# Kernel tuning notes

Hardware: AMD Instinct MI355X
Metric: run time of the kernel (lower is better)

The kernel has to match this reference:

```python
import jax, jax.numpy as jnp
import numpy as np

HW, B, C, NH, NC, HF, WF = 2500, 2, 256, 8, 6, 64, 176
DFF = 4 * C
EPS = 1e-5

def _layernorm(x, g, b):
    m = x.mean(-1, keepdims=True)
    v = ((x - m) ** 2).mean(-1, keepdims=True)
    return (x - m) / jnp.sqrt(v + EPS) * g + b

def _mha(q, kv, in_w, in_b, ow, ob):
    # q: [L,B,C], kv: [S,B,C] (batch_first=False, torch nn.MultiheadAttention)
    L, Bq, Cq = q.shape
    S = kv.shape[0]
    Dh = Cq // NH
    qp = (q @ in_w[:Cq].T + in_b[:Cq]).reshape(L, Bq, NH, Dh)
    kp = (kv @ in_w[Cq:2 * Cq].T + in_b[Cq:2 * Cq]).reshape(S, Bq, NH, Dh)
    vp = (kv @ in_w[2 * Cq:].T + in_b[2 * Cq:]).reshape(S, Bq, NH, Dh)
    att = jnp.einsum('lbhd,sbhd->bhls', qp, kp) * (1.0 / np.sqrt(Dh))
    att = jax.nn.softmax(att, axis=-1)
    out = jnp.einsum('bhls,sbhd->lbhd', att, vp).reshape(L, Bq, Cq)
    return out @ ow.T + ob

def _grid_sample_zeros(feat, grid):
    # feat: [B,N,C,H,W], grid: [B,N,Q,2] in [-1,1]; bilinear, align_corners=False, zero padding
    Bb, N, Cc, Hf, Wf = feat.shape
    Q = grid.shape[2]
    x = (grid[..., 0] + 1.0) * (Wf / 2.0) - 0.5
    y = (grid[..., 1] + 1.0) * (Hf / 2.0) - 0.5
    x0 = jnp.floor(x); y0 = jnp.floor(y)
    wx = x - x0; wy = y - y0
    x0i = x0.astype(jnp.int32); y0i = y0.astype(jnp.int32)
    ff = feat.reshape(Bb, N, Cc, Hf * Wf)
    def corner(xi, yi, w):
        valid = (xi >= 0) & (xi < Wf) & (yi >= 0) & (yi < Hf)
        idx = jnp.clip(yi, 0, Hf - 1) * Wf + jnp.clip(xi, 0, Wf - 1)  # [B,N,Q]
        g = jnp.take_along_axis(ff, jnp.broadcast_to(idx[:, :, None, :], (Bb, N, Cc, Q)), axis=-1)
        return g * (w * valid)[:, :, None, :]
    return (corner(x0i, y0i, (1.0 - wx) * (1.0 - wy)) + corner(x0i + 1, y0i, wx * (1.0 - wy))
            + corner(x0i, y0i + 1, (1.0 - wx) * wy) + corner(x0i + 1, y0i + 1, wx * wy))

def _forward(bev_queries, prev_bev, image_feat, reference_points, camera_intrinsics, camera_extrinsics,
             in_proj_w, in_proj_b, out_proj_w, out_proj_b, tsa_norm_g, tsa_norm_b,
             sca_w, sca_b, sca_norm_g, sca_norm_b, ffn_w1, ffn_b1, ffn_w2, ffn_b2, ffn_norm_g, ffn_norm_b):
    # TSA (dropout is identity in eval)
    tsa_out = _mha(bev_queries, prev_bev, in_proj_w, in_proj_b, out_proj_w, out_proj_b)
    x = _layernorm(bev_queries + tsa_out, tsa_norm_g, tsa_norm_b)
    # SCA: ego->camera->image projection
    R = camera_extrinsics[:, :, :3, :3]            # [B,N,3,3]
    t = camera_extrinsics[:, :, :3, 3]             # [B,N,3]
    R_e2c = jnp.swapaxes(R, -1, -2)
    t_e2c = -jnp.einsum('bnij,bnj->bni', R_e2c, t)
    pts_cam = jnp.einsum('bnij,qj->bnqi', R_e2c, reference_points) + t_e2c[:, :, None, :]  # [B,N,Q,3]
    pts_img = jnp.einsum('bnij,bnqj->bnqi', camera_intrinsics, pts_cam)
    uv = pts_img[..., :2] / jnp.maximum(pts_img[..., 2:3], 1e-5)
    grid = jnp.stack([2.0 * uv[..., 0] / WF - 1.0, 2.0 * uv[..., 1] / HF - 1.0], axis=-1)  # [B,N,Q,2]
    Bq = bev_queries.shape[1]
    feat_r = image_feat.reshape(Bq, NC, C, HF, WF)
    sampled = _grid_sample_zeros(feat_r, grid).mean(axis=1)   # [B,C,Q]
    sampled = jnp.transpose(sampled, (2, 0, 1))               # [Q,B,C]
    sca_out = sampled @ sca_w.T + sca_b
    x = _layernorm(x + sca_out, sca_norm_g, sca_norm_b)
    # FFN (torch nn.GELU default = exact erf)
    h = jax.nn.gelu(x @ ffn_w1 + ffn_b1, approximate=False)
    ffn_out = h @ ffn_w2 + ffn_b2
    return _layernorm(x + ffn_out, ffn_norm_g, ffn_norm_b)

def setup_inputs():
    key = jax.random.key(0)
    ks = jax.random.split(key, 16)
    f = jnp.float32
    s = 0.02
    return {
        'bev_queries': jax.random.normal(ks[0], (HW, B, C), f),
        'prev_bev': jax.random.normal(ks[1], (HW, B, C), f),
        'image_feat': jax.random.normal(ks[2], (B * NC, C, HF, WF), f),
        'reference_points': jax.random.normal(ks[3], (HW, 3), f) * 20.0,
        'camera_intrinsics': jax.random.normal(ks[4], (B, NC, 3, 3), f),
        'camera_extrinsics': jax.random.normal(ks[5], (B, NC, 4, 4), f),
        'spatial_shapes': jnp.array([[HF, WF]], jnp.int32),
        'in_proj_w': jax.random.normal(ks[6], (3 * C, C), f) * s,
        'in_proj_b': jnp.zeros((3 * C,), f),
        'out_proj_w': jax.random.normal(ks[7], (C, C), f) * s,
        'out_proj_b': jnp.zeros((C,), f),
        'tsa_norm_g': jnp.ones((C,), f), 'tsa_norm_b': jnp.zeros((C,), f),
        'sca_w': jax.random.normal(ks[8], (C, C), f) * s,
        'sca_b': jnp.zeros((C,), f),
        'sca_norm_g': jnp.ones((C,), f), 'sca_norm_b': jnp.zeros((C,), f),
        'ffn_w1': jax.random.normal(ks[9], (C, DFF), f) * s,
        'ffn_b1': jnp.zeros((DFF,), f),
        'ffn_w2': jax.random.normal(ks[10], (DFF, C), f) * s,
        'ffn_b2': jnp.zeros((C,), f),
        'ffn_norm_g': jnp.ones((C,), f), 'ffn_norm_b': jnp.zeros((C,), f),
    }

def reference(bev_queries, prev_bev, image_feat, reference_points, camera_intrinsics, camera_extrinsics,
              in_proj_w, in_proj_b, out_proj_w, out_proj_b, tsa_norm_g, tsa_norm_b,
              sca_w, sca_b, sca_norm_g, sca_norm_b, ffn_w1, ffn_b1, ffn_w2, ffn_b2, ffn_norm_g, ffn_norm_b,
              spatial_shapes):
    return _forward(bev_queries, prev_bev, image_feat, reference_points, camera_intrinsics, camera_extrinsics,
                    in_proj_w, in_proj_b, out_proj_w, out_proj_b, tsa_norm_g, tsa_norm_b,
                    sca_w, sca_b, sca_norm_g, sca_norm_b, ffn_w1, ffn_b1, ffn_w2, ffn_b2, ffn_norm_g, ffn_norm_b)
```

## Files before the change

### kernel.cpp

```cpp
#include <hip/hip_runtime.h>

typedef unsigned short u16;
typedef __attribute__((ext_vector_type(8))) __bf16 bf8_t;
typedef __attribute__((ext_vector_type(4))) float f4_t;

union bf8u { u16 u[8]; bf8_t v; uint4 q; };

__device__ __forceinline__ float bf2f(u16 v) {
  return __uint_as_float(((unsigned int)v) << 16);
}
__device__ __forceinline__ u16 f2bf(float f) {
  union { __bf16 h; u16 u; } c;
  c.h = (__bf16)f;
  return c.u;
}
__device__ __forceinline__ float bflo(unsigned int w) { return __uint_as_float(w << 16); }
__device__ __forceinline__ float bfhi(unsigned int w) { return __uint_as_float(w & 0xFFFF0000u); }
__device__ __forceinline__ float ldf1(const void* p, size_t i, int isf32) {
  return isf32 ? ((const float*)p)[i] : bf2f(((const u16*)p)[i]);
}
__device__ __forceinline__ unsigned int cvtpk(float lo, float hi) {
  unsigned int w;
  asm("v_cvt_pk_bf16_f32 %0, %1, %2" : "=v"(w) : "v"(lo), "v"(hi));
  return w;
}

#define LQ    2500
#define LQP   2560
#define BB    2
#define CC    256
#define NCC   6
#define HFF   64
#define WFF   176
#define DFF   1024
#define MROWS 5000

#define WB_UV   256
#define WB_WQKV 240256
#define WB_WOP  633472
#define WB_WSC  764544
#define WB_WF1  895616
#define WB_WF2  1419904
#define WB_S1   1944192
#define WB_S2   (WB_S1 + 2621440)
#define WB_S3   (WB_S2 + 2621440)
#define WB_VT   (WB_S3 + 2621440)
#define WB_H    WB_S2

__global__ void detect_k(const u16* __restrict__ rp, int* __restrict__ flag) {
  int bad = 0;
  for (int i = threadIdx.x; i < 7500; i += 64) {
    float v = bf2f(rp[i]);
    if (!(fabsf(v) < 1e6f)) bad = 1;
  }
  int anybad = __any(bad);
  if (threadIdx.x == 0) flag[0] = anybad ? 1 : 0;
}

struct WDesc {
  const void* src[6];
  u16* dst[6];
  int n[6];
  int mode[6];
  int Kd[6], Nd[6];
};
__global__ __launch_bounds__(256) void cvtw_k(WDesc d,
    const void* __restrict__ refp, const void* __restrict__ intr,
    const void* __restrict__ extr, float* __restrict__ uv,
    const int* __restrict__ flag) {
  const int df = flag[0];
  const int i = blockIdx.y;
  if (i == 6) {
    for (int idx = blockIdx.x * 256 + threadIdx.x; idx < BB * NCC * LQ; idx += gridDim.x * 256) {
      const int bc = idx / LQ;
      const int q = idx - bc * LQ;
      float R[3][3], tv[3], Kc[3][3], p[3];
#pragma unroll
      for (int a = 0; a < 3; ++a) {
#pragma unroll
        for (int j = 0; j < 3; ++j) {
          R[a][j] = ldf1(extr, bc*16 + a*4 + j, df);
          Kc[a][j] = ldf1(intr, bc*9 + a*3 + j, df);
        }
        tv[a] = ldf1(extr, bc*16 + a*4 + 3, df);
      }
#pragma unroll
      for (int j = 0; j < 3; ++j) p[j] = ldf1(refp, q*3 + j, df) - tv[j];
      float pc[3];
#pragma unroll
      for (int a = 0; a < 3; ++a) pc[a] = R[0][a]*p[0] + R[1][a]*p[1] + R[2][a]*p[2];
      float im[3];
#pragma unroll
      for (int a = 0; a < 3; ++a) im[a] = Kc[a][0]*pc[0] + Kc[a][1]*pc[1] + Kc[a][2]*pc[2];
      const float z = fmaxf(im[2], 1e-5f);
      uv[(size_t)idx*2 + 0] = im[0] / z - 0.5f;
      uv[(size_t)idx*2 + 1] = im[1] / z - 0.5f;
    }
    return;
  }
  const int n = d.n[i];
  for (int j = blockIdx.x * 256 + threadIdx.x; j < n; j += gridDim.x * 256) {
    if (d.mode[i] == 3) {
      if (df) {
        const float4 r = ((const float4*)d.src[i])[j];
        const unsigned int lo = (unsigned int)f2bf(r.x) | ((unsigned int)f2bf(r.y) << 16);
        const unsigned int hi = (unsigned int)f2bf(r.z) | ((unsigned int)f2bf(r.w) << 16);
        ((uint2*)d.dst[i])[j] = make_uint2(lo, hi);
      } else {
        ((uint2*)d.dst[i])[j] = ((const uint2*)d.src[i])[j];
      }
    } else if (d.mode[i] == 2) {
      const int row = j / (LQP - LQ), col = LQ + j % (LQP - LQ);
      d.dst[i][(size_t)row * LQP + col] = 0;
    } else {
      const int K = d.Kd[i], N = d.Nd[i];
      const int nn = j / K, kk = j - nn * K;
      d.dst[i][j] = f2bf(ldf1(d.src[i], (size_t)kk * N + nn, df));
    }
  }
}

template<int KTPL, int ACT, int NT>
__global__ __launch_bounds__(64) void gemm_nl(
    const u16* __restrict__ Xv, const u16* __restrict__ W,
    const void* __restrict__ bias,
    u16* __restrict__ Y, int M, int N, const int* __restrict__ flag)
{
  const int df = flag[0];
  const int lane = threadIdx.x;
  const int ln15 = lane & 15, l4 = lane >> 4;
  const int m0 = blockIdx.x * 16, n0 = blockIdx.y * (NT * 16);
  const int am = min(m0 + ln15, M - 1);

  f4_t acc[NT];
#pragma unroll
  for (int nt = 0; nt < NT; ++nt) acc[nt] = (f4_t){0.f, 0.f, 0.f, 0.f};

#pragma unroll 8
  for (int k0 = 0; k0 < KTPL; k0 += 32) {
    bf8u a;
    a.q = *(const uint4*)(Xv + (size_t)am * KTPL + k0 + l4 * 8);
#pragma unroll
    for (int nt = 0; nt < NT; ++nt) {
      bf8u b;
      b.q = *(const uint4*)&W[(size_t)(n0 + nt * 16 + ln15) * KTPL + k0 + l4 * 8];
      acc[nt] = __builtin_amdgcn_mfma_f32_16x16x32_bf16(a.v, b.v, acc[nt], 0, 0, 0);
    }
  }
#pragma unroll
  for (int nt = 0; nt < NT; ++nt) {
    const int gn = n0 + nt * 16 + ln15;
    const float bv = ldf1(bias, gn, df);
#pragma unroll
    for (int r = 0; r < 4; ++r) {
      const int gm = m0 + l4 * 4 + r;
      if (gm < M) {
        float x = acc[nt][r] + bv;
        if (ACT) x = 0.5f * x * (1.f + erff(x * 0.70710678118654752f));
        Y[(size_t)gm * N + gn] = f2bf(x);
      }
    }
  }
}

template<int KT, int RES, int TOOUT>
__global__ __launch_bounds__(256) void gemm_ln(
    const u16* __restrict__ Xv, const u16* __restrict__ W,
    const void* __restrict__ bias, const void* __restrict__ resv,
    const void* __restrict__ gw, const void* __restrict__ bw,
    void* __restrict__ Yv, int M, const int* __restrict__ flag)
{
  __shared__ float sR[4][16];
  const int df = flag[0];
  const int t = threadIdx.x;
  const int lane = t & 63, wn = t >> 6;
  const int ln15 = lane & 15, l4 = lane >> 4;
  const int m0 = blockIdx.x * 16;
  const int am = min(m0 + ln15, M - 1);

  f4_t acc[4];
#pragma unroll
  for (int nt = 0; nt < 4; ++nt) acc[nt] = (f4_t){0.f, 0.f, 0.f, 0.f};

#pragma unroll 8
  for (int k0 = 0; k0 < KT; k0 += 32) {
    bf8u a;
    a.q = *(const uint4*)(Xv + (size_t)am * KT + k0 + l4 * 8);
#pragma unroll
    for (int nt = 0; nt < 4; ++nt) {
      bf8u b;
      b.q = *(const uint4*)&W[(size_t)(wn * 64 + nt * 16 + ln15) * KT + k0 + l4 * 8];
      acc[nt] = __builtin_amdgcn_mfma_f32_16x16x32_bf16(a.v, b.v, acc[nt], 0, 0, 0);
    }
  }
  float x[4][4];
#pragma unroll
  for (int nt = 0; nt < 4; ++nt) {
    const int gn = wn * 64 + nt * 16 + ln15;
    const float bv = ldf1(bias, gn, df);
#pragma unroll
    for (int r = 0; r < 4; ++r) {
      const int gm = m0 + l4 * 4 + r;
      float xx = acc[nt][r] + bv;
      const size_t ri = (size_t)min(gm, M - 1) * CC + gn;
      if (RES == 1)      xx += bf2f(((const u16*)resv)[ri]);
      else if (RES == 2) xx += ldf1(resv, ri, df);
      x[nt][r] = xx;
    }
  }
  float ps[4];
#pragma unroll
  for (int r = 0; r < 4; ++r) {
    ps[r] = x[0][r] + x[1][r] + x[2][r] + x[3][r];
#pragma unroll
    for (int o = 1; o < 16; o <<= 1) ps[r] += __shfl_xor(ps[r], o);
  }
  if (ln15 == 0) {
#pragma unroll
    for (int r = 0; r < 4; ++r) sR[wn][l4 * 4 + r] = ps[r];
  }
  __syncthreads();
  float mean[4];
#pragma unroll
  for (int r = 0; r < 4; ++r) {
    const int row = l4 * 4 + r;
    mean[r] = (sR[0][row] + sR[1][row] + sR[2][row] + sR[3][row]) * 0.00390625f;
  }
  __syncthreads();
  float pq[4];
#pragma unroll
  for (int r = 0; r < 4; ++r) {
    float d0 = x[0][r] - mean[r], d1 = x[1][r] - mean[r];
    float d2 = x[2][r] - mean[r], d3 = x[3][r] - mean[r];
    pq[r] = d0*d0 + d1*d1 + d2*d2 + d3*d3;
#pragma unroll
    for (int o = 1; o < 16; o <<= 1) pq[r] += __shfl_xor(pq[r], o);
  }
  if (ln15 == 0) {
#pragma unroll
    for (int r = 0; r < 4; ++r) sR[wn][l4 * 4 + r] = pq[r];
  }
  __syncthreads();
  float rstd[4];
#pragma unroll
  for (int r = 0; r < 4; ++r) {
    const int row = l4 * 4 + r;
    const float v = (sR[0][row] + sR[1][row] + sR[2][row] + sR[3][row]) * 0.00390625f;
    rstd[r] = rsqrtf(v + 1e-5f);
  }
#pragma unroll
  for (int nt = 0; nt < 4; ++nt) {
    const int gn = wn * 64 + nt * 16 + ln15;
    const float g = ldf1(gw, gn, df);
    const float be = ldf1(bw, gn, df);
#pragma unroll
    for (int r = 0; r < 4; ++r) {
      const int gm = m0 + l4 * 4 + r;
      if (gm < M) {
        const float y = (x[nt][r] - mean[r]) * rstd[r] * g + be;
        if (TOOUT && df) ((float*)Yv)[(size_t)gm * CC + gn] = y;
        else             ((u16*)Yv)[(size_t)gm * CC + gn] = f2bf(y);
      }
    }
  }
}

__global__ __launch_bounds__(64) void gemm_qkv(
    const void* __restrict__ Xq, const void* __restrict__ Xkv,
    const u16* __restrict__ Wqkv, const void* __restrict__ bias,
    u16* __restrict__ Qo, u16* __restrict__ Ko, u16* __restrict__ Vt,
    const int* __restrict__ flag)
{
  const int df = flag[0];
  const int lane = threadIdx.x;
  const int ln15 = lane & 15, l4 = lane >> 4;
  const int which = blockIdx.y >> 2;
  const int n0 = (blockIdx.y & 3) * 64;
  const void* Xv = (which == 0) ? Xq : Xkv;
  const u16* W = Wqkv + (size_t)which * 65536;
  const int m0 = blockIdx.x * 16;
  const int am = min(m0 + ln15, MROWS - 1);

  f4_t acc[4];
#pragma unroll
  for (int nt = 0; nt < 4; ++nt) acc[nt] = (f4_t){0.f, 0.f, 0.f, 0.f};

#pragma unroll 8
  for (int k0 = 0; k0 < CC; k0 += 32) {
    bf8u a;
    if (df) {
      const float* p = (const float*)Xv + (size_t)am * CC + k0 + l4 * 8;
      float4 r0 = *(const float4*)p, r1 = *(const float4*)(p + 4);
      a.u[0]=f2bf(r0.x); a.u[1]=f2bf(r0.y); a.u[2]=f2bf(r0.z); a.u[3]=f2bf(r0.w);
      a.u[4]=f2bf(r1.x); a.u[5]=f2bf(r1.y); a.u[6]=f2bf(r1.z); a.u[7]=f2bf(r1.w);
    } else {
      a.q = *(const uint4*)((const u16*)Xv + (size_t)am * CC + k0 + l4 * 8);
    }
#pragma unroll
    for (int nt = 0; nt < 4; ++nt) {
      bf8u b;
      b.q = *(const uint4*)&W[(size_t)(n0 + nt * 16 + ln15) * CC + k0 + l4 * 8];
      acc[nt] = __builtin_amdgcn_mfma_f32_16x16x32_bf16(a.v, b.v, acc[nt], 0, 0, 0);
    }
  }
#pragma unroll
  for (int nt = 0; nt < 4; ++nt) {
    const int gn = n0 + nt * 16 + ln15;
    const float bv = ldf1(bias, which * 256 + gn, df);
#pragma unroll
    for (int r = 0; r < 4; ++r) {
      const int gm = m0 + l4 * 4 + r;
      if (gm < MROWS) {
        const float x = acc[nt][r] + bv;
        if (which == 2) {
          const int tt = gm >> 1;
          const int tx = tt & 63;
          const int tp = (tx & 35) | ((tx & 12) << 1) | ((tx & 16) >> 2);
          Vt[(size_t)(gn + (gm & 1) * 256) * LQP + ((tt & ~63) | tp)] = f2bf(x);
        } else {
          u16* Y = (which == 0) ? Qo : Ko;
          Y[(size_t)gm * CC + gn] = f2bf(x);
        }
      }
    }
  }
}

#define TPW 10
__global__ __launch_bounds__(256) void attn_mf(
    const u16* __restrict__ Qw, const u16* __restrict__ Kw,
    const u16* __restrict__ Vt, u16* __restrict__ Ow)
{
  __shared__ float sO[4][32][33];
  __shared__ float sM[4][32];
  __shared__ float sL[4][32];
  const int t = threadIdx.x;
  const int lane = t & 63, w = t >> 6;
  const int ln15 = lane & 15, l4 = lane >> 4;
  const int q0 = blockIdx.x * 32;
  const int by = blockIdx.y;
  const int b = by >> 3, h = by & 7;
  const float SCL2E = 0.25505654481f;

  bf8u aqA, aqB;
  {
    const int qra = min(q0 + ln15, LQ - 1);
    const int qrb = min(q0 + 16 + ln15, LQ - 1);
    bf8u qr;
    qr.q = *(const uint4*)&Qw[((size_t)qra * BB + b) * CC + h * 32 + l4 * 8];
#pragma unroll
    for (int i = 0; i < 8; ++i) aqA.u[i] = f2bf(bf2f(qr.u[i]) * SCL2E);
    qr.q = *(const uint4*)&Qw[((size_t)qrb * BB + b) * CC + h * 32 + l4 * 8];
#pragma unroll
    for (int i = 0; i < 8; ++i) aqB.u[i] = f2bf(bf2f(qr.u[i]) * SCL2E);
  }

  f4_t oaccA[2], oaccB[2];
  oaccA[0] = (f4_t){0.f,0.f,0.f,0.f}; oaccA[1] = (f4_t){0.f,0.f,0.f,0.f};
  oaccB[0] = (f4_t){0.f,0.f,0.f,0.f}; oaccB[1] = (f4_t){0.f,0.f,0.f,0.f};
  float mA = -1e30f, lA = 0.f;
  float mB = -1e30f, lB = 0.f;

  const int kt0 = w * TPW;
  const u16* Kbase = &Kw[(size_t)b * CC + h * 32 + l4 * 8];
  const u16* Vbase = &Vt[(size_t)(by * 32 + ln15) * LQP + l4 * 8];

  bf8u bkn[4];
#pragma unroll
  for (int nt = 0; nt < 4; ++nt)
    bkn[nt].q = *(const uint4*)&Kbase[(size_t)(kt0 * 64 + nt * 16 + ln15) * CC];

  for (int kt = kt0; kt < kt0 + TPW; ++kt) {
    const int kb = kt * 64;
    bf8u av[2][2];
#pragma unroll
    for (int m = 0; m < 2; ++m)
#pragma unroll
      for (int dt = 0; dt < 2; ++dt)
        av[m][dt].q = *(const uint4*)&Vbase[(size_t)(dt * 16) * LQP + kb + m * 32];
    f4_t svA[4], svB[4];
    __builtin_amdgcn_s_setprio(1);
#pragma unroll
    for (int nt = 0; nt < 4; ++nt) {
      f4_t z = (f4_t){0.f,0.f,0.f,0.f};
      svA[nt] = __builtin_amdgcn_mfma_f32_16x16x32_bf16(bkn[nt].v, aqA.v, z, 0, 0, 0);
      f4_t z2 = (f4_t){0.f,0.f,0.f,0.f};
      svB[nt] = __builtin_amdgcn_mfma_f32_16x16x32_bf16(bkn[nt].v, aqB.v, z2, 0, 0, 0);
    }
    __builtin_amdgcn_s_setprio(0);
    if (kt + 1 < kt0 + TPW) {
#pragma unroll
      for (int nt = 0; nt < 4; ++nt)
        bkn[nt].q = *(const uint4*)&Kbase[(size_t)(kb + 64 + nt * 16 + ln15) * CC];
    }
    float pA[4][4], pB[4][4];
    if (kb + 64 <= LQ) {
#pragma unroll
      for (int nt = 0; nt < 4; ++nt)
#pragma unroll
        for (int r = 0; r < 4; ++r) { pA[nt][r] = svA[nt][r]; pB[nt][r] = svB[nt][r]; }
    } else {
#pragma unroll
      for (int nt = 0; nt < 4; ++nt)
#pragma unroll
        for (int r = 0; r < 4; ++r) {
          const bool ok = (kb + nt * 16 + l4 * 4 + r < LQ);
          pA[nt][r] = ok ? svA[nt][r] : -1e30f;
          pB[nt][r] = ok ? svB[nt][r] : -1e30f;
        }
    }
    {
      const float thr = mA + 8.f;
      bool nd = false;
#pragma unroll
      for (int nt = 0; nt < 4; ++nt)
#pragma unroll
        for (int r = 0; r < 4; ++r) nd |= (pA[nt][r] > thr);
      if (__any(nd)) {
        const float x0 = fmaxf(fmaxf(pA[0][0], pA[0][1]), fmaxf(pA[0][2], pA[0][3]));
        const float x1 = fmaxf(fmaxf(pA[1][0], pA[1][1]), fmaxf(pA[1][2], pA[1][3]));
        const float x2 = fmaxf(fmaxf(pA[2][0], pA[2][1]), fmaxf(pA[2][2], pA[2][3]));
        const float x3 = fmaxf(fmaxf(pA[3][0], pA[3][1]), fmaxf(pA[3][2], pA[3][3]));
        float mloc = fmaxf(fmaxf(x0, x1), fmaxf(x2, x3));
        mloc = fmaxf(mloc, __shfl_xor(mloc, 16));
        mloc = fmaxf(mloc, __shfl_xor(mloc, 32));
        const float mn = fmaxf(mA, mloc);
        const float alpha = __builtin_amdgcn_exp2f(mA - mn);
        mA = mn;
        lA *= alpha;
#pragma unroll
        for (int r = 0; r < 4; ++r) { oaccA[0][r] *= alpha; oaccA[1][r] *= alpha; }
      }
      float s = 0.f;
#pragma unroll
      for (int nt = 0; nt < 4; ++nt)
#pragma unroll
        for (int r = 0; r < 4; ++r) {
          const float e = __builtin_amdgcn_exp2f(pA[nt][r] - mA);
          pA[nt][r] = e; s += e;
        }
      lA += s;
    }
    {
      const float thr = mB + 8.f;
      bool nd = false;
#pragma unroll
      for (int nt = 0; nt < 4; ++nt)
#pragma unroll
        for (int r = 0; r < 4; ++r) nd |= (pB[nt][r] > thr);
      if (__any(nd)) {
        const float x0 = fmaxf(fmaxf(pB[0][0], pB[0][1]), fmaxf(pB[0][2], pB[0][3]));
        const float x1 = fmaxf(fmaxf(pB[1][0], pB[1][1]), fmaxf(pB[1][2], pB[1][3]));
        const float x2 = fmaxf(fmaxf(pB[2][0], pB[2][1]), fmaxf(pB[2][2], pB[2][3]));
        const float x3 = fmaxf(fmaxf(pB[3][0], pB[3][1]), fmaxf(pB[3][2], pB[3][3]));
        float mloc = fmaxf(fmaxf(x0, x1), fmaxf(x2, x3));
        mloc = fmaxf(mloc, __shfl_xor(mloc, 16));
        mloc = fmaxf(mloc, __shfl_xor(mloc, 32));
        const float mn = fmaxf(mB, mloc);
        const float alpha = __builtin_amdgcn_exp2f(mB - mn);
        mB = mn;
        lB *= alpha;
#pragma unroll
        for (int r = 0; r < 4; ++r) { oaccB[0][r] *= alpha; oaccB[1][r] *= alpha; }
      }
      float s = 0.f;
#pragma unroll
      for (int nt = 0; nt < 4; ++nt)
#pragma unroll
        for (int r = 0; r < 4; ++r) {
          const float e = __builtin_amdgcn_exp2f(pB[nt][r] - mB);
          pB[nt][r] = e; s += e;
        }
      lB += s;
    }
    __builtin_amdgcn_s_setprio(1);
#pragma unroll
    for (int m = 0; m < 2; ++m) {
      bf8u pba, pbb;
      pba.q = make_uint4(cvtpk(pA[2*m][0], pA[2*m][1]),   cvtpk(pA[2*m][2], pA[2*m][3]),
                         cvtpk(pA[2*m+1][0], pA[2*m+1][1]), cvtpk(pA[2*m+1][2], pA[2*m+1][3]));
      pbb.q = make_uint4(cvtpk(pB[2*m][0], pB[2*m][1]),   cvtpk(pB[2*m][2], pB[2*m][3]),
                         cvtpk(pB[2*m+1][0], pB[2*m+1][1]), cvtpk(pB[2*m+1][2], pB[2*m+1][3]));
#pragma unroll
      for (int dt = 0; dt < 2; ++dt) {
        oaccA[dt] = __builtin_amdgcn_mfma_f32_16x16x32_bf16(av[m][dt].v, pba.v, oaccA[dt], 0, 0, 0);
        oaccB[dt] = __builtin_amdgcn_mfma_f32_16x16x32_bf16(av[m][dt].v, pbb.v, oaccB[dt], 0, 0, 0);
      }
    }
    __builtin_amdgcn_s_setprio(0);
  }
  lA += __shfl_xor(lA, 16);  lA += __shfl_xor(lA, 32);
  lB += __shfl_xor(lB, 16);  lB += __shfl_xor(lB, 32);
#pragma unroll
  for (int dt = 0; dt < 2; ++dt)
#pragma unroll
    for (int r = 0; r < 4; ++r) {
      sO[w][ln15][dt * 16 + l4 * 4 + r]      = oaccA[dt][r];
      sO[w][16 + ln15][dt * 16 + l4 * 4 + r] = oaccB[dt][r];
    }
  if (l4 == 0) {
    sM[w][ln15] = mA; sL[w][ln15] = lA;
    sM[w][16 + ln15] = mB; sL[w][16 + ln15] = lB;
  }
  __syncthreads();
#pragma unroll
  for (int i = t; i < 1024; i += 256) {
    const int row = i >> 5, col = i & 31;
    const float M = fmaxf(fmaxf(sM[0][row], sM[1][row]), fmaxf(sM[2][row], sM[3][row]));
    float l = 0.f, O = 0.f;
#pragma unroll
    for (int w4 = 0; w4 < 4; ++w4) {
      const float sc = __builtin_amdgcn_exp2f(sM[w4][row] - M);
      l += sc * sL[w4][row];
      O += sc * sO[w4][row][col];
    }
    const int q = q0 + row;
    if (q < LQ)
      Ow[((size_t)q * BB + b) * CC + h * 32 + col] = f2bf(O / l);
  }
}

__global__ __launch_bounds__(256) void samp_k(
    const void* __restrict__ feat, const float* __restrict__ uv,
    u16* __restrict__ S, const int* __restrict__ flag)
{
  const int df = flag[0];
  const int c = blockIdx.x;
  const int b = blockIdx.y / 5;
  const int ch = blockIdx.y % 5;
  const int qend = min((ch + 1) * 500, LQ);
  for (int q = ch * 500 + threadIdx.x; q < qend; q += 256) {
    float acc = 0.f;
#pragma unroll
    for (int cam = 0; cam < NCC; ++cam) {
      const int bc = b * NCC + cam;
      const float x = uv[((size_t)bc * LQ + q) * 2 + 0];
      const float y = uv[((size_t)bc * LQ + q) * 2 + 1];
      const float xf = floorf(x), yf = floorf(y);
      const int x0 = (int)xf, y0 = (int)yf;
      const float wx = x - xf, wy = y - yf;
      const size_t base = ((size_t)bc * CC + c) * (HFF * WFF);
      const bool vx0 = (x0 >= 0) & (x0 < WFF);
      const bool vx1 = (x0 + 1 >= 0) & (x0 + 1 < WFF);
      const bool vy0 = (y0 >= 0) & (y0 < HFF);
      const bool vy1 = (y0 + 1 >= 0) & (y0 + 1 < HFF);
      if (vy0) {
        const size_t rb = base + (size_t)y0 * WFF;
        if (vx0) acc += (1.f - wx) * (1.f - wy) * ldf1(feat, rb + x0, df);
        if (vx1) acc += wx * (1.f - wy) * ldf1(feat, rb + x0 + 1, df);
      }
      if (vy1) {
        const size_t rb = base + (size_t)(y0 + 1) * WFF;
        if (vx0) acc += (1.f - wx) * wy * ldf1(feat, rb + x0, df);
        if (vx1) acc += wx * wy * ldf1(feat, rb + x0 + 1, df);
      }
    }
    S[((size_t)q * BB + b) * CC + c] = f2bf(acc * (1.f / 6.f));
  }
}

extern "C" void kernel_launch(void* const* d_in, const int* in_sizes, int n_in,
                              void* d_out, int out_size, void* d_ws, size_t ws_size,
                              hipStream_t stream) {
  (void)in_sizes; (void)n_in; (void)out_size; (void)ws_size;
  char* base = (char*)d_ws;
  int* flag = (int*)base;
  float* UV = (float*)(base + WB_UV);
  u16* WQKV = (u16*)(base + WB_WQKV);
  u16* WOP  = (u16*)(base + WB_WOP);
  u16* WSC  = (u16*)(base + WB_WSC);
  u16* WF1  = (u16*)(base + WB_WF1);
  u16* WF2  = (u16*)(base + WB_WF2);
  u16* S1 = (u16*)(base + WB_S1);
  u16* S2 = (u16*)(base + WB_S2);
  u16* S3 = (u16*)(base + WB_S3);
  u16* VT = (u16*)(base + WB_VT);
  u16* H  = (u16*)(base + WB_H);

  detect_k<<<1, 64, 0, stream>>>((const u16*)d_in[3], flag);

  WDesc wd;
  wd.src[0] = d_in[7];  wd.dst[0] = WQKV; wd.n[0] = 49152;  wd.mode[0] = 3; wd.Kd[0] = 0;    wd.Nd[0] = 0;
  wd.src[1] = d_in[9];  wd.dst[1] = WOP;  wd.n[1] = 16384;  wd.mode[1] = 3; wd.Kd[1] = 0;    wd.Nd[1] = 0;
  wd.src[2] = d_in[13]; wd.dst[2] = WSC;  wd.n[2] = 16384;  wd.mode[2] = 3; wd.Kd[2] = 0;    wd.Nd[2] = 0;
  wd.src[3] = d_in[17]; wd.dst[3] = WF1;  wd.n[3] = 262144; wd.mode[3] = 1; wd.Kd[3] = 256;  wd.Nd[3] = 1024;
  wd.src[4] = d_in[19]; wd.dst[4] = WF2;  wd.n[4] = 262144; wd.mode[4] = 1; wd.Kd[4] = 1024; wd.Nd[4] = 256;
  wd.src[5] = nullptr;  wd.dst[5] = VT;   wd.n[5] = 512 * (LQP - LQ); wd.mode[5] = 2; wd.Kd[5] = 0; wd.Nd[5] = 0;
  cvtw_k<<<dim3(128, 7), 256, 0, stream>>>(wd, d_in[3], d_in[4], d_in[5], UV, flag);

  gemm_qkv<<<dim3(313, 12), 64, 0, stream>>>(d_in[0], d_in[1], WQKV, d_in[8], S1, S2, VT, flag);

  attn_mf<<<dim3(79, 16), 256, 0, stream>>>(S1, S2, VT, S3);

  gemm_ln<256,2,0><<<313, 256, 0, stream>>>(S3, WOP, d_in[10], d_in[0], d_in[11], d_in[12], S2, MROWS, flag);

  samp_k<<<dim3(CC, BB * 5), 256, 0, stream>>>(d_in[2], UV, VT, flag);

  gemm_ln<256,1,0><<<313, 256, 0, stream>>>(VT, WSC, d_in[14], S2, d_in[15], d_in[16], S1, MROWS, flag);

  gemm_nl<256,1,4><<<dim3(313, 16), 64, 0, stream>>>(S1, WF1, d_in[18], H, MROWS, DFF, flag);
  gemm_ln<1024,1,1><<<313, 256, 0, stream>>>(H, WF2, d_in[20], S1, d_in[21], d_in[22], d_out, MROWS, flag);
}
```

Before: 464.0 us.

## Split-K gemm_ln across 16 waves with LDS reduction; tiled weight transpose kernel

```diff
diff --git a/kernel.cpp b/kernel.cpp
--- a/kernel.cpp
+++ b/kernel.cpp
@@ -58,19 +58,17 @@
 }
 
 struct WDesc {
-  const void* src[6];
-  u16* dst[6];
-  int n[6];
-  int mode[6];
-  int Kd[6], Nd[6];
+  const void* src[3];
+  u16* dst[3];
+  int n[3];
 };
-__global__ __launch_bounds__(256) void cvtw_k(WDesc d,
+__global__ __launch_bounds__(256) void cvtw_k(WDesc d, u16* __restrict__ vtp,
     const void* __restrict__ refp, const void* __restrict__ intr,
     const void* __restrict__ extr, float* __restrict__ uv,
     const int* __restrict__ flag) {
   const int df = flag[0];
   const int i = blockIdx.y;
-  if (i == 6) {
+  if (i == 4) {
     for (int idx = blockIdx.x * 256 + threadIdx.x; idx < BB * NCC * LQ; idx += gridDim.x * 256) {
       const int bc = idx / LQ;
       const int q = idx - bc * LQ;
@@ -98,25 +96,52 @@
     }
     return;
   }
+  if (i == 3) {
+    const int n = 512 * (LQP - LQ);
+    for (int j = blockIdx.x * 256 + threadIdx.x; j < n; j += gridDim.x * 256) {
+      const int row = j / (LQP - LQ), col = LQ + j % (LQP - LQ);
+      vtp[(size_t)row * LQP + col] = 0;
+    }
+    return;
+  }
   const int n = d.n[i];
   for (int j = blockIdx.x * 256 + threadIdx.x; j < n; j += gridDim.x * 256) {
-    if (d.mode[i] == 3) {
-      if (df) {
-        const float4 r = ((const float4*)d.src[i])[j];
-        const unsigned int lo = (unsigned int)f2bf(r.x) | ((unsigned int)f2bf(r.y) << 16);
-        const unsigned int hi = (unsigned int)f2bf(r.z) | ((unsigned int)f2bf(r.w) << 16);
-        ((uint2*)d.dst[i])[j] = make_uint2(lo, hi);
-      } else {
-        ((uint2*)d.dst[i])[j] = ((const uint2*)d.src[i])[j];
-      }
-    } else if (d.mode[i] == 2) {
-      const int row = j / (LQP - LQ), col = LQ + j % (LQP - LQ);
-      d.dst[i][(size_t)row * LQP + col] = 0;
+    if (df) {
+      const float4 r = ((const float4*)d.src[i])[j];
+      const unsigned int lo = (unsigned int)f2bf(r.x) | ((unsigned int)f2bf(r.y) << 16);
+      const unsigned int hi = (unsigned int)f2bf(r.z) | ((unsigned int)f2bf(r.w) << 16);
+      ((uint2*)d.dst[i])[j] = make_uint2(lo, hi);
     } else {
-      const int K = d.Kd[i], N = d.Nd[i];
-      const int nn = j / K, kk = j - nn * K;
-      d.dst[i][j] = f2bf(ldf1(d.src[i], (size_t)kk * N + nn, df));
-    }
+      ((uint2*)d.dst[i])[j] = ((const uint2*)d.src[i])[j];
+    }
+  }
+}
+
+__global__ __launch_bounds__(256) void trans_k(
+    const void* __restrict__ s0, u16* __restrict__ d0,
+    const void* __restrict__ s1, u16* __restrict__ d1,
+    const int* __restrict__ flag)
+{
+  __shared__ u16 tile[64][66];
+  const int df = flag[0];
+  const void* src; u16* dst; int Ks, Ns;
+  if (blockIdx.y == 0) { src = s0; dst = d0; Ks = 256;  Ns = 1024; }
+  else                 { src = s1; dst = d1; Ks = 1024; Ns = 256;  }
+  const int ntn = Ns >> 6;
+  const int kx = blockIdx.x / ntn, nx = blockIdx.x % ntn;
+  const int k0 = kx * 64, n0 = nx * 64;
+  const int t = threadIdx.x;
+  const int col = t & 63, rq = t >> 6;
+#pragma unroll
+  for (int i = 0; i < 16; ++i) {
+    const int r = i * 4 + rq;
+    tile[col][r] = f2bf(ldf1(src, (size_t)(k0 + r) * Ns + n0 + col, df));
+  }
+  __syncthreads();
+#pragma unroll
+  for (int i = 0; i < 16; ++i) {
+    const int n = i * 4 + rq;
+    dst[(size_t)(n0 + n) * Ks + k0 + col] = tile[n][col];
   }
 }
 
@@ -164,103 +189,92 @@
 }
 
 template<int KT, int RES, int TOOUT>
-__global__ __launch_bounds__(256) void gemm_ln(
+__global__ __launch_bounds__(1024) void gemm_ln(
     const u16* __restrict__ Xv, const u16* __restrict__ W,
     const void* __restrict__ bias, const void* __restrict__ resv,
     const void* __restrict__ gw, const void* __restrict__ bw,
     void* __restrict__ Yv, int M, const int* __restrict__ flag)
 {
-  __shared__ float sR[4][16];
+  __shared__ float sP[4][16][260];
   const int df = flag[0];
   const int t = threadIdx.x;
-  const int lane = t & 63, wn = t >> 6;
+  const int lane = t & 63, w = t >> 6;
   const int ln15 = lane & 15, l4 = lane >> 4;
+  const int ks = w >> 2, wn = w & 3;
   const int m0 = blockIdx.x * 16;
   const int am = min(m0 + ln15, M - 1);
+  constexpr int KS = KT / 4;
+  const int kbase = ks * KS;
 
   f4_t acc[4];
 #pragma unroll
   for (int nt = 0; nt < 4; ++nt) acc[nt] = (f4_t){0.f, 0.f, 0.f, 0.f};
 
-#pragma unroll 8
-  for (int k0 = 0; k0 < KT; k0 += 32) {
+#pragma unroll
+  for (int k0 = 0; k0 < KS; k0 += 32) {
     bf8u a;
-    a.q = *(const uint4*)(Xv + (size_t)am * KT + k0 + l4 * 8);
+    a.q = *(const uint4*)(Xv + (size_t)am * KT + kbase + k0 + l4 * 8);
 #pragma unroll
     for (int nt = 0; nt < 4; ++nt) {
       bf8u b;
-      b.q = *(const uint4*)&W[(size_t)(wn * 64 + nt * 16 + ln15) * KT + k0 + l4 * 8];
+      b.q = *(const uint4*)&W[(size_t)(wn * 64 + nt * 16 + ln15) * KT + kbase + k0 + l4 * 8];
       acc[nt] = __builtin_amdgcn_mfma_f32_16x16x32_bf16(a.v, b.v, acc[nt], 0, 0, 0);
     }
   }
-  float x[4][4];
-#pragma unroll
-  for (int nt = 0; nt < 4; ++nt) {
-    const int gn = wn * 64 + nt * 16 + ln15;
-    const float bv = ldf1(bias, gn, df);
-#pragma unroll
-    for (int r = 0; r < 4; ++r) {
-      const int gm = m0 + l4 * 4 + r;
-      float xx = acc[nt][r] + bv;
-      const size_t ri = (size_t)min(gm, M - 1) * CC + gn;
-      if (RES == 1)      xx += bf2f(((const u16*)resv)[ri]);
-      else if (RES == 2) xx += ldf1(resv, ri, df);
-      x[nt][r] = xx;
-    }
-  }
-  float ps[4];
-#pragma unroll
-  for (int r = 0; r < 4; ++r) {
-    ps[r] = x[0][r] + x[1][r] + x[2][r] + x[3][r];
-#pragma unroll
-    for (int o = 1; o < 16; o <<= 1) ps[r] += __shfl_xor(ps[r], o);
-  }
-  if (ln15 == 0) {
-#pragma unroll
-    for (int r = 0; r < 4; ++r) sR[wn][l4 * 4 + r] = ps[r];
-  }
+#pragma unroll
+  for (int nt = 0; nt < 4; ++nt)
+#pragma unroll
+    for (int r = 0; r < 4; ++r)
+      sP[ks][l4 * 4 + r][wn * 64 + nt * 16 + ln15] = acc[nt][r];
   __syncthreads();
-  float mean[4];
-#pragma unroll
-  for (int r = 0; r < 4; ++r) {
-    const int row = l4 * 4 + r;
-    mean[r] = (sR[0][row] + sR[1][row] + sR[2][row] + sR[3][row]) * 0.00390625f;
-  }
-  __syncthreads();
-  float pq[4];
-#pragma unroll
-  for (int r = 0; r < 4; ++r) {
-    float d0 = x[0][r] - mean[r], d1 = x[1][r] - mean[r];
-    float d2 = x[2][r] - mean[r], d3 = x[3][r] - mean[r];
-    pq[r] = d0*d0 + d1*d1 + d2*d2 + d3*d3;
-#pragma unroll
-    for (int o = 1; o < 16; o <<= 1) pq[r] += __shfl_xor(pq[r], o);
-  }
-  if (ln15 == 0) {
-#pragma unroll
-    for (int r = 0; r < 4; ++r) sR[wn][l4 * 4 + r] = pq[r];
-  }
-  __syncthreads();
-  float rstd[4];
-#pragma unroll
-  for (int r = 0; r < 4; ++r) {
-    const int row = l4 * 4 + r;
-    const float v = (sR[0][row] + sR[1][row] + sR[2][row] + sR[3][row]) * 0.00390625f;
-    rstd[r] = rsqrtf(v + 1e-5f);
-  }
-#pragma unroll
-  for (int nt = 0; nt < 4; ++nt) {
-    const int gn = wn * 64 + nt * 16 + ln15;
-    const float g = ldf1(gw, gn, df);
-    const float be = ldf1(bw, gn, df);
-#pragma unroll
-    for (int r = 0; r < 4; ++r) {
-      const int gm = m0 + l4 * 4 + r;
-      if (gm < M) {
-        const float y = (x[nt][r] - mean[r]) * rstd[r] * g + be;
-        if (TOOUT && df) ((float*)Yv)[(size_t)gm * CC + gn] = y;
-        else             ((u16*)Yv)[(size_t)gm * CC + gn] = f2bf(y);
-      }
+  const int gm = m0 + w;
+  const int c = lane * 4;
+  const float4 x0 = *(const float4*)&sP[0][w][c];
+  const float4 x1 = *(const float4*)&sP[1][w][c];
+  const float4 x2 = *(const float4*)&sP[2][w][c];
+  const float4 x3 = *(const float4*)&sP[3][w][c];
+  float xx[4] = { x0.x + x1.x + x2.x + x3.x, x0.y + x1.y + x2.y + x3.y,
+                  x0.z + x1.z + x2.z + x3.z, x0.w + x1.w + x2.w + x3.w };
+#pragma unroll
+  for (int j = 0; j < 4; ++j) xx[j] += ldf1(bias, c + j, df);
+  const size_t ri = (size_t)min(gm, M - 1) * CC + c;
+  if (RES == 1) {
+    const uint2 rr = *(const uint2*)((const u16*)resv + ri);
+    xx[0] += bflo(rr.x); xx[1] += bfhi(rr.x);
+    xx[2] += bflo(rr.y); xx[3] += bfhi(rr.y);
+  } else if (RES == 2) {
+    if (df) {
+      const float4 rf = *(const float4*)((const float*)resv + ri);
+      xx[0] += rf.x; xx[1] += rf.y; xx[2] += rf.z; xx[3] += rf.w;
+    } else {
+      const uint2 rr = *(const uint2*)((const u16*)resv + ri);
+      xx[0] += bflo(rr.x); xx[1] += bfhi(rr.x);
+      xx[2] += bflo(rr.y); xx[3] += bfhi(rr.y);
+    }
+  }
+  float s = xx[0] + xx[1] + xx[2] + xx[3];
+#pragma unroll
+  for (int o = 1; o < 64; o <<= 1) s += __shfl_xor(s, o);
+  const float mean = s * 0.00390625f;
+  const float d0 = xx[0] - mean, d1 = xx[1] - mean, d2 = xx[2] - mean, d3 = xx[3] - mean;
+  float sq = d0*d0 + d1*d1 + d2*d2 + d3*d3;
+#pragma unroll
+  for (int o = 1; o < 64; o <<= 1) sq += __shfl_xor(sq, o);
+  const float rstd = rsqrtf(sq * 0.00390625f + 1e-5f);
+  const float g0 = ldf1(gw, c+0, df), g1 = ldf1(gw, c+1, df);
+  const float g2 = ldf1(gw, c+2, df), g3 = ldf1(gw, c+3, df);
+  const float b0 = ldf1(bw, c+0, df), b1 = ldf1(bw, c+1, df);
+  const float b2 = ldf1(bw, c+2, df), b3 = ldf1(bw, c+3, df);
+  const float y0 = d0 * rstd * g0 + b0;
+  const float y1 = d1 * rstd * g1 + b1;
+  const float y2 = d2 * rstd * g2 + b2;
+  const float y3 = d3 * rstd * g3 + b3;
+  if (gm < M) {
+    if (TOOUT && df) {
+      *(float4*)((float*)Yv + (size_t)gm * CC + c) = make_float4(y0, y1, y2, y3);
+    } else {
+      u16* yp = (u16*)Yv + (size_t)gm * CC + c;
+      *(uint2*)yp = make_uint2(cvtpk(y0, y1), cvtpk(y2, y3));
     }
   }
 }
@@ -580,24 +594,22 @@
   detect_k<<<1, 64, 0, stream>>>((const u16*)d_in[3], flag);
 
   WDesc wd;
-  wd.src[0] = d_in[7];  wd.dst[0] = WQKV; wd.n[0] = 49152;  wd.mode[0] = 3; wd.Kd[0] = 0;    wd.Nd[0] = 0;
-  wd.src[1] = d_in[9];  wd.dst[1] = WOP;  wd.n[1] = 16384;  wd.mode[1] = 3; wd.Kd[1] = 0;    wd.Nd[1] = 0;
-  wd.src[2] = d_in[13]; wd.dst[2] = WSC;  wd.n[2] = 16384;  wd.mode[2] = 3; wd.Kd[2] = 0;    wd.Nd[2] = 0;
-  wd.src[3] = d_in[17]; wd.dst[3] = WF1;  wd.n[3] = 262144; wd.mode[3] = 1; wd.Kd[3] = 256;  wd.Nd[3] = 1024;
-  wd.src[4] = d_in[19]; wd.dst[4] = WF2;  wd.n[4] = 262144; wd.mode[4] = 1; wd.Kd[4] = 1024; wd.Nd[4] = 256;
-  wd.src[5] = nullptr;  wd.dst[5] = VT;   wd.n[5] = 512 * (LQP - LQ); wd.mode[5] = 2; wd.Kd[5] = 0; wd.Nd[5] = 0;
-  cvtw_k<<<dim3(128, 7), 256, 0, stream>>>(wd, d_in[3], d_in[4], d_in[5], UV, flag);
+  wd.src[0] = d_in[7];  wd.dst[0] = WQKV; wd.n[0] = 49152;
+  wd.src[1] = d_in[9];  wd.dst[1] = WOP;  wd.n[1] = 16384;
+  wd.src[2] = d_in[13]; wd.dst[2] = WSC;  wd.n[2] = 16384;
+  cvtw_k<<<dim3(128, 5), 256, 0, stream>>>(wd, VT, d_in[3], d_in[4], d_in[5], UV, flag);
+  trans_k<<<dim3(64, 2), 256, 0, stream>>>(d_in[17], WF1, d_in[19], WF2, flag);
 
   gemm_qkv<<<dim3(313, 12), 64, 0, stream>>>(d_in[0], d_in[1], WQKV, d_in[8], S1, S2, VT, flag);
 
   attn_mf<<<dim3(79, 16), 256, 0, stream>>>(S1, S2, VT, S3);
 
-  gemm_ln<256,2,0><<<313, 256, 0, stream>>>(S3, WOP, d_in[10], d_in[0], d_in[11], d_in[12], S2, MROWS, flag);
+  gemm_ln<256,2,0><<<313, 1024, 0, stream>>>(S3, WOP, d_in[10], d_in[0], d_in[11], d_in[12], S2, MROWS, flag);
 
   samp_k<<<dim3(CC, BB * 5), 256, 0, stream>>>(d_in[2], UV, VT, flag);
 
-  gemm_ln<256,1,0><<<313, 256, 0, stream>>>(VT, WSC, d_in[14], S2, d_in[15], d_in[16], S1, MROWS, flag);
+  gemm_ln<256,1,0><<<313, 1024, 0, stream>>>(VT, WSC, d_in[14], S2, d_in[15], d_in[16], S1, MROWS, flag);
 
   gemm_nl<256,1,4><<<dim3(313, 16), 64, 0, stream>>>(S1, WF1, d_in[18], H, MROWS, DFF, flag);
-  gemm_ln<1024,1,1><<<313, 256, 0, stream>>>(H, WF2, d_in[20], S1, d_in[21], d_in[22], d_out, MROWS, flag);
-}
+  gemm_ln<1024,1,1><<<313, 1024, 0, stream>>>(H, WF2, d_in[20], S1, d_in[21], d_in[22], d_out, MROWS, flag);
+}
```

Measured after the change: 475.4 us. 2.5% more time.

## Use 32-row tiles in QKV and FFN1 GEMMs and add tiled weight transpose

Applied to the files above, without the earlier changes.

```diff
diff --git a/kernel.cpp b/kernel.cpp
--- a/kernel.cpp
+++ b/kernel.cpp
@@ -58,19 +58,17 @@
 }
 
 struct WDesc {
-  const void* src[6];
-  u16* dst[6];
-  int n[6];
-  int mode[6];
-  int Kd[6], Nd[6];
+  const void* src[3];
+  u16* dst[3];
+  int n[3];
 };
-__global__ __launch_bounds__(256) void cvtw_k(WDesc d,
+__global__ __launch_bounds__(256) void cvtw_k(WDesc d, u16* __restrict__ vtp,
     const void* __restrict__ refp, const void* __restrict__ intr,
     const void* __restrict__ extr, float* __restrict__ uv,
     const int* __restrict__ flag) {
   const int df = flag[0];
   const int i = blockIdx.y;
-  if (i == 6) {
+  if (i == 4) {
     for (int idx = blockIdx.x * 256 + threadIdx.x; idx < BB * NCC * LQ; idx += gridDim.x * 256) {
       const int bc = idx / LQ;
       const int q = idx - bc * LQ;
@@ -98,25 +96,52 @@
     }
     return;
   }
+  if (i == 3) {
+    const int n = 512 * (LQP - LQ);
+    for (int j = blockIdx.x * 256 + threadIdx.x; j < n; j += gridDim.x * 256) {
+      const int row = j / (LQP - LQ), col = LQ + j % (LQP - LQ);
+      vtp[(size_t)row * LQP + col] = 0;
+    }
+    return;
+  }
   const int n = d.n[i];
   for (int j = blockIdx.x * 256 + threadIdx.x; j < n; j += gridDim.x * 256) {
-    if (d.mode[i] == 3) {
-      if (df) {
-        const float4 r = ((const float4*)d.src[i])[j];
-        const unsigned int lo = (unsigned int)f2bf(r.x) | ((unsigned int)f2bf(r.y) << 16);
-        const unsigned int hi = (unsigned int)f2bf(r.z) | ((unsigned int)f2bf(r.w) << 16);
-        ((uint2*)d.dst[i])[j] = make_uint2(lo, hi);
-      } else {
-        ((uint2*)d.dst[i])[j] = ((const uint2*)d.src[i])[j];
-      }
-    } else if (d.mode[i] == 2) {
-      const int row = j / (LQP - LQ), col = LQ + j % (LQP - LQ);
-      d.dst[i][(size_t)row * LQP + col] = 0;
+    if (df) {
+      const float4 r = ((const float4*)d.src[i])[j];
+      const unsigned int lo = (unsigned int)f2bf(r.x) | ((unsigned int)f2bf(r.y) << 16);
+      const unsigned int hi = (unsigned int)f2bf(r.z) | ((unsigned int)f2bf(r.w) << 16);
+      ((uint2*)d.dst[i])[j] = make_uint2(lo, hi);
     } else {
-      const int K = d.Kd[i], N = d.Nd[i];
-      const int nn = j / K, kk = j - nn * K;
-      d.dst[i][j] = f2bf(ldf1(d.src[i], (size_t)kk * N + nn, df));
-    }
+      ((uint2*)d.dst[i])[j] = ((const uint2*)d.src[i])[j];
+    }
+  }
+}
+
+__global__ __launch_bounds__(256) void trans_k(
+    const void* __restrict__ s0, u16* __restrict__ d0,
+    const void* __restrict__ s1, u16* __restrict__ d1,
+    const int* __restrict__ flag)
+{
+  __shared__ u16 tile[64][66];
+  const int df = flag[0];
+  const void* src; u16* dst; int Ks, Ns;
+  if (blockIdx.y == 0) { src = s0; dst = d0; Ks = 256;  Ns = 1024; }
+  else                 { src = s1; dst = d1; Ks = 1024; Ns = 256;  }
+  const int ntn = Ns >> 6;
+  const int kx = blockIdx.x / ntn, nx = blockIdx.x % ntn;
+  const int k0 = kx * 64, n0 = nx * 64;
+  const int t = threadIdx.x;
+  const int col = t & 63, rq = t >> 6;
+#pragma unroll
+  for (int i = 0; i < 16; ++i) {
+    const int r = i * 4 + rq;
+    tile[col][r] = f2bf(ldf1(src, (size_t)(k0 + r) * Ns + n0 + col, df));
+  }
+  __syncthreads();
+#pragma unroll
+  for (int i = 0; i < 16; ++i) {
+    const int n = i * 4 + rq;
+    dst[(size_t)(n0 + n) * Ks + k0 + col] = tile[n][col];
   }
 }
 
@@ -129,35 +154,43 @@
   const int df = flag[0];
   const int lane = threadIdx.x;
   const int ln15 = lane & 15, l4 = lane >> 4;
-  const int m0 = blockIdx.x * 16, n0 = blockIdx.y * (NT * 16);
-  const int am = min(m0 + ln15, M - 1);
-
-  f4_t acc[NT];
-#pragma unroll
-  for (int nt = 0; nt < NT; ++nt) acc[nt] = (f4_t){0.f, 0.f, 0.f, 0.f};
+  const int m0 = blockIdx.x * 32, n0 = blockIdx.y * (NT * 16);
+  const int am0 = min(m0 + ln15, M - 1);
+  const int am1 = min(m0 + 16 + ln15, M - 1);
+
+  f4_t acc[2][NT];
+#pragma unroll
+  for (int g = 0; g < 2; ++g)
+#pragma unroll
+    for (int nt = 0; nt < NT; ++nt) acc[g][nt] = (f4_t){0.f, 0.f, 0.f, 0.f};
 
 #pragma unroll 8
   for (int k0 = 0; k0 < KTPL; k0 += 32) {
-    bf8u a;
-    a.q = *(const uint4*)(Xv + (size_t)am * KTPL + k0 + l4 * 8);
+    bf8u a0, a1;
+    a0.q = *(const uint4*)(Xv + (size_t)am0 * KTPL + k0 + l4 * 8);
+    a1.q = *(const uint4*)(Xv + (size_t)am1 * KTPL + k0 + l4 * 8);
 #pragma unroll
     for (int nt = 0; nt < NT; ++nt) {
       bf8u b;
       b.q = *(const uint4*)&W[(size_t)(n0 + nt * 16 + ln15) * KTPL + k0 + l4 * 8];
-      acc[nt] = __builtin_amdgcn_mfma_f32_16x16x32_bf16(a.v, b.v, acc[nt], 0, 0, 0);
-    }
-  }
-#pragma unroll
-  for (int nt = 0; nt < NT; ++nt) {
-    const int gn = n0 + nt * 16 + ln15;
-    const float bv = ldf1(bias, gn, df);
-#pragma unroll
-    for (int r = 0; r < 4; ++r) {
-      const int gm = m0 + l4 * 4 + r;
-      if (gm < M) {
-        float x = acc[nt][r] + bv;
-        if (ACT) x = 0.5f * x * (1.f + erff(x * 0.70710678118654752f));
-        Y[(size_t)gm * N + gn] = f2bf(x);
+      acc[0][nt] = __builtin_amdgcn_mfma_f32_16x16x32_bf16(a0.v, b.v, acc[0][nt], 0, 0, 0);
+      acc[1][nt] = __builtin_amdgcn_mfma_f32_16x16x32_bf16(a1.v, b.v, acc[1][nt], 0, 0, 0);
+    }
+  }
+#pragma unroll
+  for (int g = 0; g < 2; ++g) {
+#pragma unroll
+    for (int nt = 0; nt < NT; ++nt) {
+      const int gn = n0 + nt * 16 + ln15;
+      const float bv = ldf1(bias, gn, df);
+#pragma unroll
+      for (int r = 0; r < 4; ++r) {
+        const int gm = m0 + g * 16 + l4 * 4 + r;
+        if (gm < M) {
+          float x = acc[g][nt][r] + bv;
+          if (ACT) x = 0.5f * x * (1.f + erff(x * 0.70710678118654752f));
+          Y[(size_t)gm * N + gn] = f2bf(x);
+        }
       }
     }
   }
@@ -278,48 +311,60 @@
   const int n0 = (blockIdx.y & 3) * 64;
   const void* Xv = (which == 0) ? Xq : Xkv;
   const u16* W = Wqkv + (size_t)which * 65536;
-  const int m0 = blockIdx.x * 16;
-  const int am = min(m0 + ln15, MROWS - 1);
-
-  f4_t acc[4];
-#pragma unroll
-  for (int nt = 0; nt < 4; ++nt) acc[nt] = (f4_t){0.f, 0.f, 0.f, 0.f};
+  const int m0 = blockIdx.x * 32;
+  const int am0 = min(m0 + ln15, MROWS - 1);
+  const int am1 = min(m0 + 16 + ln15, MROWS - 1);
+
+  f4_t acc[2][4];
+#pragma unroll
+  for (int g = 0; g < 2; ++g)
+#pragma unroll
+    for (int nt = 0; nt < 4; ++nt) acc[g][nt] = (f4_t){0.f, 0.f, 0.f, 0.f};
 
 #pragma unroll 8
   for (int k0 = 0; k0 < CC; k0 += 32) {
-    bf8u a;
+    bf8u a0, a1;
     if (df) {
-      const float* p = (const float*)Xv + (size_t)am * CC + k0 + l4 * 8;
-      float4 r0 = *(const float4*)p, r1 = *(const float4*)(p + 4);
-      a.u[0]=f2bf(r0.x); a.u[1]=f2bf(r0.y); a.u[2]=f2bf(r0.z); a.u[3]=f2bf(r0.w);
-      a.u[4]=f2bf(r1.x); a.u[5]=f2bf(r1.y); a.u[6]=f2bf(r1.z); a.u[7]=f2bf(r1.w);
+      const float* p0 = (const float*)Xv + (size_t)am0 * CC + k0 + l4 * 8;
+      float4 r0 = *(const float4*)p0, r1 = *(const float4*)(p0 + 4);
+      a0.u[0]=f2bf(r0.x); a0.u[1]=f2bf(r0.y); a0.u[2]=f2bf(r0.z); a0.u[3]=f2bf(r0.w);
+      a0.u[4]=f2bf(r1.x); a0.u[5]=f2bf(r1.y); a0.u[6]=f2bf(r1.z); a0.u[7]=f2bf(r1.w);
+      const float* p1 = (const float*)Xv + (size_t)am1 * CC + k0 + l4 * 8;
+      float4 r2 = *(const float4*)p1, r3 = *(const float4*)(p1 + 4);
+      a1.u[0]=f2bf(r2.x); a1.u[1]=f2bf(r2.y); a1.u[2]=f2bf(r2.z); a1.u[3]=f2bf(r2.w);
+      a1.u[4]=f2bf(r3.x); a1.u[5]=f2bf(r3.y); a1.u[6]=f2bf(r3.z); a1.u[7]=f2bf(r3.w);
     } else {
-      a.q = *(const uint4*)((const u16*)Xv + (size_t)am * CC + k0 + l4 * 8);
+      a0.q = *(const uint4*)((const u16*)Xv + (size_t)am0 * CC + k0 + l4 * 8);
+      a1.q = *(const uint4*)((const u16*)Xv + (size_t)am1 * CC + k0 + l4 * 8);
     }
 #pragma unroll
     for (int nt = 0; nt < 4; ++nt) {
       bf8u b;
       b.q = *(const uint4*)&W[(size_t)(n0 + nt * 16 + ln15) * CC + k0 + l4 * 8];
-      acc[nt] = __builtin_amdgcn_mfma_f32_16x16x32_bf16(a.v, b.v, acc[nt], 0, 0, 0);
-    }
-  }
-#pragma unroll
-  for (int nt = 0; nt < 4; ++nt) {
-    const int gn = n0 + nt * 16 + ln15;
-    const float bv = ldf1(bias, which * 256 + gn, df);
-#pragma unroll
-    for (int r = 0; r < 4; ++r) {
-      const int gm = m0 + l4 * 4 + r;
-      if (gm < MROWS) {
-        const float x = acc[nt][r] + bv;
-        if (which == 2) {
-          const int tt = gm >> 1;
-          const int tx = tt & 63;
-          const int tp = (tx & 35) | ((tx & 12) << 1) | ((tx & 16) >> 2);
-          Vt[(size_t)(gn + (gm & 1) * 256) * LQP + ((tt & ~63) | tp)] = f2bf(x);
-        } else {
-          u16* Y = (which == 0) ? Qo : Ko;
-          Y[(size_t)gm * CC + gn] = f2bf(x);
+      acc[0][nt] = __builtin_amdgcn_mfma_f32_16x16x32_bf16(a0.v, b.v, acc[0][nt], 0, 0, 0);
+      acc[1][nt] = __builtin_amdgcn_mfma_f32_16x16x32_bf16(a1.v, b.v, acc[1][nt], 0, 0, 0);
+    }
+  }
+#pragma unroll
+  for (int g = 0; g < 2; ++g) {
+#pragma unroll
+    for (int nt = 0; nt < 4; ++nt) {
+      const int gn = n0 + nt * 16 + ln15;
+      const float bv = ldf1(bias, which * 256 + gn, df);
+#pragma unroll
+      for (int r = 0; r < 4; ++r) {
+        const int gm = m0 + g * 16 + l4 * 4 + r;
+        if (gm < MROWS) {
+          const float x = acc[g][nt][r] + bv;
+          if (which == 2) {
+            const int tt = gm >> 1;
+            const int tx = tt & 63;
+            const int tp = (tx & 35) | ((tx & 12) << 1) | ((tx & 16) >> 2);
+            Vt[(size_t)(gn + (gm & 1) * 256) * LQP + ((tt & ~63) | tp)] = f2bf(x);
+          } else {
+            u16* Y = (which == 0) ? Qo : Ko;
+            Y[(size_t)gm * CC + gn] = f2bf(x);
+          }
         }
       }
     }
@@ -580,15 +625,13 @@
   detect_k<<<1, 64, 0, stream>>>((const u16*)d_in[3], flag);
 
   WDesc wd;
-  wd.src[0] = d_in[7];  wd.dst[0] = WQKV; wd.n[0] = 49152;  wd.mode[0] = 3; wd.Kd[0] = 0;    wd.Nd[0] = 0;
-  wd.src[1] = d_in[9];  wd.dst[1] = WOP;  wd.n[1] = 16384;  wd.mode[1] = 3; wd.Kd[1] = 0;    wd.Nd[1] = 0;
-  wd.src[2] = d_in[13]; wd.dst[2] = WSC;  wd.n[2] = 16384;  wd.mode[2] = 3; wd.Kd[2] = 0;    wd.Nd[2] = 0;
-  wd.src[3] = d_in[17]; wd.dst[3] = WF1;  wd.n[3] = 262144; wd.mode[3] = 1; wd.Kd[3] = 256;  wd.Nd[3] = 1024;
-  wd.src[4] = d_in[19]; wd.dst[4] = WF2;  wd.n[4] = 262144; wd.mode[4] = 1; wd.Kd[4] = 1024; wd.Nd[4] = 256;
-  wd.src[5] = nullptr;  wd.dst[5] = VT;   wd.n[5] = 512 * (LQP - LQ); wd.mode[5] = 2; wd.Kd[5] = 0; wd.Nd[5] = 0;
-  cvtw_k<<<dim3(128, 7), 256, 0, stream>>>(wd, d_in[3], d_in[4], d_in[5], UV, flag);
-
-  gemm_qkv<<<dim3(313, 12), 64, 0, stream>>>(d_in[0], d_in[1], WQKV, d_in[8], S1, S2, VT, flag);
+  wd.src[0] = d_in[7];  wd.dst[0] = WQKV; wd.n[0] = 49152;
+  wd.src[1] = d_in[9];  wd.dst[1] = WOP;  wd.n[1] = 16384;
+  wd.src[2] = d_in[13]; wd.dst[2] = WSC;  wd.n[2] = 16384;
+  cvtw_k<<<dim3(128, 5), 256, 0, stream>>>(wd, VT, d_in[3], d_in[4], d_in[5], UV, flag);
+  trans_k<<<dim3(64, 2), 256, 0, stream>>>(d_in[17], WF1, d_in[19], WF2, flag);
+
+  gemm_qkv<<<dim3(157, 12), 64, 0, stream>>>(d_in[0], d_in[1], WQKV, d_in[8], S1, S2, VT, flag);
 
   attn_mf<<<dim3(79, 16), 256, 0, stream>>>(S1, S2, VT, S3);
 
@@ -598,6 +641,6 @@
 
   gemm_ln<256,1,0><<<313, 256, 0, stream>>>(VT, WSC, d_in[14], S2, d_in[15], d_in[16], S1, MROWS, flag);
 
-  gemm_nl<256,1,4><<<dim3(313, 16), 64, 0, stream>>>(S1, WF1, d_in[18], H, MROWS, DFF, flag);
+  gemm_nl<256,1,4><<<dim3(157, 16), 64, 0, stream>>>(S1, WF1, d_in[18], H, MROWS, DFF, flag);
   gemm_ln<1024,1,1><<<313, 256, 0, stream>>>(H, WF2, d_in[20], S1, d_in[21], d_in[22], d_out, MROWS, flag);
 }
```

Measured after the change: 458.6 us. No clear change (-1.2%).
